# Optimization experiments

Hardware: AMD Instinct MI355X
Metric: run time of the kernel (lower is better)

Reference implementation:

```python
import jax, jax.numpy as jnp
import numpy as np

B, N, F_IN = 32, 512, 64
HEADS = (8, 8)
HIDS = (64, 64)
EDGE_P = 0.05  # graph density
NEG_SLOPE = 0.2
NEG_INF = -1e20


def setup_inputs() -> dict:
    key = jax.random.key(0)
    ks = jax.random.split(key, 8)
    x = jax.random.normal(ks[0], (B, N, F_IN), dtype=jnp.float32)
    adj = (jax.random.uniform(ks[1], (B, N, N)) < EDGE_P).astype(jnp.float32)
    adj = jnp.maximum(adj, adj.transpose(0, 2, 1))  # symmetric adjacency
    # mask = (batch, row): every (b, n) pair gets the masked softmax
    b_idx = jnp.repeat(jnp.arange(B, dtype=jnp.int32), N)   # [B*N]
    r_idx = jnp.tile(jnp.arange(N, dtype=jnp.int32), B)     # [B*N]
    # layer 0: f_in=64 -> f_out=64, H=8 ; layer 1: f_in=64*8=512 -> f_out=64, H=8
    W0 = jax.random.normal(ks[2], (F_IN, HIDS[0]), dtype=jnp.float32) / jnp.sqrt(jnp.float32(F_IN))
    a_src0 = jax.random.normal(ks[3], (HIDS[0], HEADS[0]), dtype=jnp.float32) / jnp.sqrt(jnp.float32(HIDS[0]))
    a_dst0 = jax.random.normal(ks[4], (HIDS[0], HEADS[0]), dtype=jnp.float32) / jnp.sqrt(jnp.float32(HIDS[0]))
    f_in1 = HIDS[0] * HEADS[0]
    W1 = jax.random.normal(ks[5], (f_in1, HIDS[1]), dtype=jnp.float32) / jnp.sqrt(jnp.float32(f_in1))
    a_src1 = jax.random.normal(ks[6], (HIDS[1], HEADS[1]), dtype=jnp.float32) / jnp.sqrt(jnp.float32(HIDS[1]))
    a_dst1 = jax.random.normal(ks[7], (HIDS[1], HEADS[1]), dtype=jnp.float32) / jnp.sqrt(jnp.float32(HIDS[1]))
    return dict(x=x, adj=adj, b_idx=b_idx, r_idx=r_idx,
                W0=W0, a_src0=a_src0, a_dst0=a_dst0,
                W1=W1, a_src1=a_src1, a_dst1=a_dst1)


def _gat_layer(x, adj, b_idx, r_idx, W, a_src, a_dst):
    # x: [B,N,f_in], adj: [B,N,N] (diag already set), W: [f_in,F], a_*: [F,H]
    hp = x @ W                                        # [B,N,F]
    s = jnp.einsum('bnf,fh->bhn', hp, a_src)          # attn_src
    d = jnp.einsum('bnf,fh->bhn', hp, a_dst)          # attn_dst
    attn = s[:, :, :, None] + d[:, :, None, :]        # [B,H,N,N]
    attn = jnp.where(attn >= 0, attn, NEG_SLOPE * attn)  # leaky_relu(0.2)
    attn = jnp.where(adj[:, None, :, :] == 0, 0.0, attn)  # masked_fill(adj==0, 0)
    rows = attn[b_idx, :, r_idx, :]                   # [K,H,N]
    rows = jnp.where(rows == 0.0, NEG_INF, rows)
    rows = jax.nn.softmax(rows, axis=-1)
    attn = attn.at[b_idx, :, r_idx, :].set(rows)
    return jnp.einsum('bhij,bjf->bhif', attn, hp)     # [B,H,N,F]


def reference(x, adj, b_idx, r_idx, W0, a_src0, a_dst0, W1, a_src1, a_dst1):
    Bn, Nn = x.shape[:2]
    # torch mutates adj in place: adj[batch,row,row] = 1 (self loops)
    adj = adj.at[b_idx, r_idx, r_idx].set(1.0)
    o = _gat_layer(x, adj, b_idx, r_idx, W0, a_src0, a_dst0)      # [B,H,N,F0]
    x1 = jax.nn.elu(o.transpose(0, 2, 1, 3).reshape(Bn, Nn, -1))  # [B,N,H*F0]
    o2 = _gat_layer(x1, adj, b_idx, r_idx, W1, a_src1, a_dst1)    # [B,H,N,F1]
    return o2.mean(axis=1)                                        # [B,N,F1]
```

## Files before the change

### kernel.cpp

```cpp
#include <hip/hip_runtime.h>
#include <hip/hip_bf16.h>
#include <math.h>

#define BB 32
#define NN 512

typedef _Float16 f16x8 __attribute__((ext_vector_type(8)));
typedef __fp16  fp16x2 __attribute__((ext_vector_type(2)));
typedef float f32x4 __attribute__((ext_vector_type(4)));

#define MFMA16(a, b, c) __builtin_amdgcn_mfma_f32_16x16x32_f16(a, b, c, 0, 0, 0)

union AF { f16x8 v; unsigned int u[4]; };

__device__ __forceinline__ void gload_lds16(const void* g, void* l) {
    __builtin_amdgcn_global_load_lds(
        (const __attribute__((address_space(1))) unsigned int*)g,
        (__attribute__((address_space(3))) unsigned int*)l, 16, 0, 0);
}
__device__ __forceinline__ void gload_lds4(const void* g, void* l) {
    __builtin_amdgcn_global_load_lds(
        (const __attribute__((address_space(1))) unsigned int*)g,
        (__attribute__((address_space(3))) unsigned int*)l, 4, 0, 0);
}

static __device__ __forceinline__ void epi16(
    const float* ctile, const float* asd_f, int row0, int t,
    float* __restrict__ s, float* __restrict__ dTg, _Float16* __restrict__ hpT,
    float* dmax_lds, float* __restrict__ pmax_out)
{
    int b = row0 >> 9, jb = row0 & 511;
    if (t < 128) {
        int rr = t >> 3, h = t & 7;
        float sv = 0.f, dv = 0.f;
#pragma unroll
        for (int f = 0; f < 64; ++f) {
            float hv = ctile[rr * 66 + f];
            sv = fmaf(hv, asd_f[f * 8 + h], sv);
            dv = fmaf(hv, asd_f[512 + f * 8 + h], dv);
        }
        s[((size_t)b * NN + jb + rr) * 8 + h] = sv;
        dTg[((size_t)b * 8 + h) * NN + jb + rr] = dv;
        dmax_lds[t] = dv;
    } else if (t < 256) {
        int t2 = t - 128;
        int f = t2 >> 1, jl = (t2 & 1) * 8;
        f16x8 hv;
#pragma unroll
        for (int e = 0; e < 8; ++e)
            hv[e] = (_Float16)ctile[(jl + e) * 66 + f];
        *(f16x8*)(hpT + ((size_t)b * 64 + f) * NN + jb + jl) = hv;
    }
    __syncthreads();
    if (t < 8) {
        float m = dmax_lds[t];
#pragma unroll
        for (int k = 1; k < 16; ++k) m = fmaxf(m, dmax_lds[t + 8 * k]);
        pmax_out[((size_t)b * 32 + (jb >> 4)) * 8 + t] = m;
    }
}

static __device__ __forceinline__ void epi32(
    const float* ctile, const float* asd_f, int row0, int t,
    float* __restrict__ s, float* __restrict__ dTg, _Float16* __restrict__ hpT,
    float* dmax_lds, float* __restrict__ pmax_out)
{
    int b = row0 >> 9, jb = row0 & 511;
    if (t < 256) {
        int rr = t >> 3, h = t & 7;
        float sv = 0.f, dv = 0.f;
#pragma unroll
        for (int f = 0; f < 64; ++f) {
            float hv = ctile[rr * 66 + f];
            sv = fmaf(hv, asd_f[f * 8 + h], sv);
            dv = fmaf(hv, asd_f[512 + f * 8 + h], dv);
        }
        s[((size_t)b * NN + jb + rr) * 8 + h] = sv;
        dTg[((size_t)b * 8 + h) * NN + jb + rr] = dv;
        dmax_lds[t] = dv;
    } else {
        int t2 = t - 256;
        int f = t2 >> 2, jl = (t2 & 3) * 8;
        f16x8 hv;
#pragma unroll
        for (int e = 0; e < 8; ++e)
            hv[e] = (_Float16)ctile[(jl + e) * 66 + f];
        *(f16x8*)(hpT + ((size_t)b * 64 + f) * NN + jb + jl) = hv;
    }
    __syncthreads();
    if (t < 8) {
        float m = dmax_lds[t];
#pragma unroll
        for (int k = 1; k < 32; ++k) m = fmaxf(m, dmax_lds[t + 8 * k]);
        pmax_out[((size_t)b * 16 + (jb >> 5)) * 8 + t] = m;
    }
}

__global__ __launch_bounds__(256) void k_front(
    const float* __restrict__ x, const float* __restrict__ W0,
    const float* __restrict__ W1, _Float16* __restrict__ W1T,
    const float* __restrict__ a_src, const float* __restrict__ a_dst,
    float* __restrict__ s, float* __restrict__ dTg, _Float16* __restrict__ hpT,
    float* __restrict__ pmax)
{
    __shared__ float ctile[16 * 66];
    __shared__ float asd_f[1024];
    __shared__ float dmax[128];
    int t = threadIdx.x, row0 = blockIdx.x * 16;
    int lane = t & 63, w = t >> 6, cn = lane & 15, rq = lane >> 4;

    if (blockIdx.x < 16) {
        int task = blockIdx.x * 256 + t;
        int n = task & 63, gabs = task >> 6;
        int c = gabs >> 3, g = gabs & 7;
        f16x8 hv;
#pragma unroll
        for (int e = 0; e < 8; ++e)
            hv[e] = (_Float16)W1[(size_t)(gabs * 8 + e) * 64 + n];
        *(f16x8*)(W1T + (size_t)n * 512 + c * 64 + (g ^ (n & 7)) * 8) = hv;
    }

    ((float4*)asd_f)[t] = (t < 128) ? ((const float4*)a_src)[t]
                                    : ((const float4*)a_dst)[t - 128];
    f32x4 acc;
#pragma unroll
    for (int e = 0; e < 4; ++e) acc[e] = 0.f;
    int nn0 = w * 16 + cn;
#pragma unroll
    for (int ks = 0; ks < 2; ++ks) {
        const float* xp = x + (size_t)(row0 + cn) * 64 + ks * 32 + rq * 8;
        float4 x0 = *(const float4*)xp, x1 = *(const float4*)(xp + 4);
        f16x8 ah = {(_Float16)x0.x, (_Float16)x0.y, (_Float16)x0.z, (_Float16)x0.w,
                    (_Float16)x1.x, (_Float16)x1.y, (_Float16)x1.z, (_Float16)x1.w};
        f16x8 bh;
#pragma unroll
        for (int e = 0; e < 8; ++e)
            bh[e] = (_Float16)W0[(size_t)((ks * 4 + rq) * 8 + e) * 64 + nn0];
        acc = MFMA16(ah, bh, acc);
    }
#pragma unroll
    for (int r = 0; r < 4; ++r)
        ctile[(rq * 4 + r) * 66 + w * 16 + cn] = acc[r];
    __syncthreads();
    epi16(ctile, asd_f, row0, t, s, dTg, hpT, dmax, pmax);
}

#define PBUILD(AOUT, SV, C0, CB, AVv, REL, DDv, Ev, Ebv)                \
    do {                                                                \
        _Pragma("unroll")                                               \
        for (int e = 0; e < 8; e += 2) {                                \
            float pA[2];                                                \
            _Pragma("unroll")                                           \
            for (int q = 0; q < 2; ++q) {                               \
                int ee = e + q;                                         \
                bool con = (AVv[ee] != 0.f) || (ee == (REL));           \
                float e0 = SV + DDv[ee];                                \
                float p0 = (e0 >= 0.f) ? (C0) * Ev[ee] : (CB) * Ebv[ee];\
                pA[q] = (con && e0 != 0.f) ? p0 : 0.f;                  \
            }                                                           \
            fp16x2 ka = __builtin_amdgcn_cvt_pkrtz(pA[0], pA[1]);       \
            AOUT.u[e >> 1] = __builtin_bit_cast(unsigned int, ka);      \
        }                                                               \
    } while (0)

template<int MODE>
__global__ __launch_bounds__(512, 4) void k_attn_fused(
    const float* __restrict__ s, const float* __restrict__ dTg,
    const float* __restrict__ pmaxd, const _Float16* __restrict__ hpT,
    const float* __restrict__ adj,
    const _Float16* __restrict__ W1T,
    const float* __restrict__ a_src, const float* __restrict__ a_dst,
    float* __restrict__ s_out, float* __restrict__ dTg_out,
    _Float16* __restrict__ hpT_out, float* __restrict__ pmax_out,
    float* __restrict__ o_f)
{
    __shared__ __align__(16) char smem[40960];
    char* bufP = smem;
    char* bufQ = smem + 18432;

    int blk = blockIdx.x;
    int vb = ((blk & 7) << 6) | (blk >> 3);
    int b = vb >> 4, i0 = (vb & 15) << 5;
    int row0 = vb * 32;
    int t = threadIdx.x, lane = t & 63, w = t >> 6;
    int cn = lane & 15, rq = lane >> 4;
    int myrow = i0 + cn;

    const _Float16* hb = hpT + (size_t)b * 64 * NN;
    int f0 = t >> 3, g0 = t & 7;
    const _Float16* hsrc = hb + (size_t)f0 * NN + ((g0 ^ (f0 & 7)) * 8);
    const float* dsrc = dTg + ((size_t)b * 8 + w) * NN + lane;
    int ar = t >> 4, ag = t & 15;
    const float* asrc = adj + (size_t)(row0 + ar) * NN + (((ag ^ (ar & 7))) << 2);

#define STAGE(BUF, JC)                                                   \
    do {                                                                 \
        gload_lds16(hsrc + (JC), (_Float16*)(BUF) + (w << 9));           \
        gload_lds4(dsrc + (JC), (float*)((BUF) + 8192) + (w << 6));      \
        gload_lds16(asrc + (JC), (float*)((BUF) + 10240) + (w << 8));    \
    } while (0)

    STAGE(bufP, 0);

    constexpr int NT = (MODE == 0) ? 32 : 16;
    float md = pmaxd[((size_t)b * NT + (lane & (NT - 1))) * 8 + w];
#pragma unroll
    for (int off = NT >> 1; off; off >>= 1) md = fmaxf(md, __shfl_xor(md, off));

    float svA = s[((size_t)b * NN + myrow) * 8 + w];
    float svB = s[((size_t)b * NN + myrow + 16) * 8 + w];
    float MA = fmaxf(svA + md, 0.f);
    float MB = fmaxf(svB + md, 0.f);
    float c0A = __expf(svA + md - MA), cbA = __expf(0.2f * (svA + md) - MA);
    float c0B = __expf(svB + md - MB), cbB = __expf(0.2f * (svB + md) - MB);
    int rq8 = rq * 8;

    f16x8 ones;
#pragma unroll
    for (int e = 0; e < 8; ++e) ones[e] = (_Float16)1.0f;

    f32x4 accA[4], accB[4], accrsA, accrsB;
#pragma unroll
    for (int e = 0; e < 4; ++e) { accrsA[e] = 0.f; accrsB[e] = 0.f; }
#pragma unroll
    for (int ft = 0; ft < 4; ++ft)
#pragma unroll
        for (int e = 0; e < 4; ++e) { accA[ft][e] = 0.f; accB[ft][e] = 0.f; }

    __syncthreads();

    for (int jcx = 0; jcx < 8; ++jcx) {
        int jc = jcx * 64;
        char* cur = (jcx & 1) ? bufQ : bufP;
        char* nxt = (jcx & 1) ? bufP : bufQ;
        if (jcx < 7) STAGE(nxt, jc + 64);
        const _Float16* hTc = (const _Float16*)cur;
        const float* ddl = (const float*)(cur + 8192) + (w << 6);
        const float* adl = (const float*)(cur + 10240);
        const float* arA = adl + cn * 64;
        const float* arB = adl + (16 + cn) * 64;
        int xA = cn & 7;
        float* Et = (float*)(smem + 36864) + (w << 7);
        {
            float ddj = ddl[lane];
            Et[lane]      = __expf(ddj - md);
            Et[lane + 64] = __expf(0.2f * (ddj - md));
        }
        asm volatile("s_waitcnt lgkmcnt(0)" ::: "memory");
#pragma unroll
        for (int ks = 0; ks < 2; ++ks) {
            int jo = ks * 32 + rq8;
            float dd[8], avA[8], avB[8], Ev[8], Ebv[8];
            *(float4*)&dd[0] = *(const float4*)(ddl + jo);
            *(float4*)&dd[4] = *(const float4*)(ddl + jo + 4);
            *(float4*)&Ev[0]  = *(const float4*)(Et + jo);
            *(float4*)&Ev[4]  = *(const float4*)(Et + jo + 4);
            *(float4*)&Ebv[0] = *(const float4*)(Et + 64 + jo);
            *(float4*)&Ebv[4] = *(const float4*)(Et + 64 + jo + 4);
            int G0 = jo >> 2;
            *(float4*)&avA[0] = *(const float4*)(arA + ((G0 ^ xA) << 2));
            *(float4*)&avA[4] = *(const float4*)(arA + (((G0 + 1) ^ xA) << 2));
            *(float4*)&avB[0] = *(const float4*)(arB + ((G0 ^ xA) << 2));
            *(float4*)&avB[4] = *(const float4*)(arB + (((G0 + 1) ^ xA) << 2));
            int relA = myrow - (jc + jo);
            int relB = relA + 16;
            AF aA, aB;
            PBUILD(aA, svA, c0A, cbA, avA, relA, dd, Ev, Ebv);
            PBUILD(aB, svB, c0B, cbB, avB, relB, dd, Ev, Ebv);
            __builtin_amdgcn_s_setprio(1);
            accrsA = MFMA16(aA.v, ones, accrsA);
            accrsB = MFMA16(aB.v, ones, accrsB);
#pragma unroll
            for (int ft = 0; ft < 4; ++ft) {
                int f = ft * 16 + cn;
                f16x8 bh = *(const f16x8*)&hTc[f * 64 + (((ks * 4 + rq) ^ (f & 7)) * 8)];
                accA[ft] = MFMA16(aA.v, bh, accA[ft]);
                accB[ft] = MFMA16(aB.v, bh, accB[ft]);
            }
            __builtin_amdgcn_s_setprio(0);
        }
        __syncthreads();
    }
#undef STAGE

    float invrA[4], invrB[4];
#pragma unroll
    for (int r = 0; r < 4; ++r) {
        invrA[r] = 1.0f / accrsA[r];
        invrB[r] = 1.0f / accrsB[r];
    }

    if (MODE == 0) {
        _Float16* x1all = (_Float16*)smem;
#pragma unroll
        for (int rt = 0; rt < 2; ++rt)
#pragma unroll
            for (int ft = 0; ft < 4; ++ft)
#pragma unroll
                for (int r = 0; r < 4; ++r) {
                    int il = rt * 16 + rq * 4 + r;
                    float v = rt ? accB[ft][r] * invrB[r]
                                 : accA[ft][r] * invrA[r];
                    v = v > 0.f ? v : __expf(v) - 1.f;
                    int f = ft * 16 + cn;
                    x1all[w * 2048 + il * 64 + (((f >> 3) ^ (il & 7)) * 8) + (f & 7)] =
                        (_Float16)v;
                }
        __syncthreads();
        f32x4 g1A, g1B;
#pragma unroll
        for (int e = 0; e < 4; ++e) { g1A[e] = 0.f; g1B[e] = 0.f; }
        int nn = (w & 3) * 16 + cn, kh = w >> 2;
        const _Float16* wb = W1T + (size_t)nn * 512;
#pragma unroll
        for (int kc2 = 0; kc2 < 4; ++kc2) {
            int kc = kh * 4 + kc2;
#pragma unroll
            for (int ks = 0; ks < 2; ++ks) {
                f16x8 bh = *(const f16x8*)(wb + kc * 64 +
                                           (((ks * 4 + rq) ^ (nn & 7)) * 8));
                f16x8 ahA = *(const f16x8*)&x1all[kc * 2048 + cn * 64 +
                                                  (((ks * 4 + rq) ^ (cn & 7)) * 8)];
                f16x8 ahB = *(const f16x8*)&x1all[kc * 2048 + (16 + cn) * 64 +
                                                  (((ks * 4 + rq) ^ (cn & 7)) * 8)];
                g1A = MFMA16(ahA, bh, g1A);
                g1B = MFMA16(ahB, bh, g1B);
            }
        }
        __syncthreads();
        float* ct = (float*)smem;
        float* asd_f = (float*)(smem + 33280);
        float* dmax = (float*)(smem + 37376);
#pragma unroll
        for (int r = 0; r < 4; ++r) {
            ct[kh * 2112 + (rq * 4 + r) * 66 + nn] = g1A[r];
            ct[kh * 2112 + (16 + rq * 4 + r) * 66 + nn] = g1B[r];
        }
        if (t < 256)
            ((float4*)asd_f)[t] = (t < 128) ? ((const float4*)a_src)[t]
                                            : ((const float4*)a_dst)[t - 128];
        __syncthreads();
        for (int idx = t; idx < 2112; idx += 512) ct[idx] += ct[2112 + idx];
        __syncthreads();
        epi32(ct, asd_f, row0, t, s_out, dTg_out, hpT_out, dmax, pmax_out);
    } else {
        float* red = (float*)smem;
#pragma unroll
        for (int ph = 0; ph < 2; ++ph) {
            if ((w >> 2) == ph) {
#pragma unroll
                for (int rt = 0; rt < 2; ++rt)
#pragma unroll
                    for (int ft = 0; ft < 4; ++ft)
#pragma unroll
                        for (int r = 0; r < 4; ++r) {
                            int il = rt * 16 + rq * 4 + r;
                            float v = rt ? accB[ft][r] * invrB[r]
                                         : accA[ft][r] * invrA[r];
                            int off = (w & 3) * 2048 + il * 64 + ft * 16 + cn;
                            if (ph == 0) red[off] = v;
                            else         red[off] += v;
                        }
            }
            __syncthreads();
        }
#pragma unroll
        for (int u = 0; u < 4; ++u) {
            int idx = t + u * 512;
            int il = idx >> 6, f = idx & 63;
            float sum = red[il * 64 + f] + red[2048 + il * 64 + f]
                      + red[4096 + il * 64 + f] + red[6144 + il * 64 + f];
            o_f[((size_t)b * NN + i0 + il) * 64 + f] = sum * 0.125f;
        }
    }
}

extern "C" void kernel_launch(void* const* d_in, const int* in_sizes, int n_in,
                              void* d_out, int out_size, void* d_ws, size_t ws_size,
                              hipStream_t stream) {
    const float* x      = (const float*)d_in[0];
    const float* adj    = (const float*)d_in[1];
    const float* W0     = (const float*)d_in[4];
    const float* a_src0 = (const float*)d_in[5];
    const float* a_dst0 = (const float*)d_in[6];
    const float* W1     = (const float*)d_in[7];
    const float* a_src1 = (const float*)d_in[8];
    const float* a_dst1 = (const float*)d_in[9];
    float* out = (float*)d_out;

    float* ws = (float*)d_ws;
    const size_t R = (size_t)BB * NN;
    const size_t BHN = (size_t)BB * 8 * NN;
    float* s0    = ws;
    float* dTg0  = s0 + R * 8;
    float* s1    = dTg0 + BHN;
    float* dTg1  = s1 + R * 8;
    float* pmax0 = dTg1 + BHN;
    float* pmax1 = pmax0 + 8192;
    _Float16* hp0T = (_Float16*)(pmax1 + 4096);
    _Float16* hp1T = hp0T + (size_t)BB * 64 * NN;
    _Float16* W1T  = hp1T + (size_t)BB * 64 * NN;

    k_front<<<1024, 256, 0, stream>>>(x, W0, W1, W1T, a_src0, a_dst0,
                                      s0, dTg0, hp0T, pmax0);
    k_attn_fused<0><<<512, 512, 0, stream>>>(s0, dTg0, pmax0, hp0T, adj,
                                             W1T, a_src1, a_dst1,
                                             s1, dTg1, hp1T, pmax1, nullptr);
    k_attn_fused<1><<<512, 512, 0, stream>>>(s1, dTg1, pmax1, hp1T, adj,
                                             nullptr, nullptr, nullptr,
                                             nullptr, nullptr, nullptr, nullptr, out);
}
```

Before: 153.3 us.

## Replace LDS double-buffered staging with direct global loads in attention kernel

```diff
diff --git a/kernel.cpp b/kernel.cpp
--- a/kernel.cpp
+++ b/kernel.cpp
@@ -12,17 +12,6 @@
 #define MFMA16(a, b, c) __builtin_amdgcn_mfma_f32_16x16x32_f16(a, b, c, 0, 0, 0)
 
 union AF { f16x8 v; unsigned int u[4]; };
-
-__device__ __forceinline__ void gload_lds16(const void* g, void* l) {
-    __builtin_amdgcn_global_load_lds(
-        (const __attribute__((address_space(1))) unsigned int*)g,
-        (__attribute__((address_space(3))) unsigned int*)l, 16, 0, 0);
-}
-__device__ __forceinline__ void gload_lds4(const void* g, void* l) {
-    __builtin_amdgcn_global_load_lds(
-        (const __attribute__((address_space(1))) unsigned int*)g,
-        (__attribute__((address_space(3))) unsigned int*)l, 4, 0, 0);
-}
 
 static __device__ __forceinline__ void epi16(
     const float* ctile, const float* asd_f, int row0, int t,
@@ -175,8 +164,6 @@
     float* __restrict__ o_f)
 {
     __shared__ __align__(16) char smem[40960];
-    char* bufP = smem;
-    char* bufQ = smem + 18432;
 
     int blk = blockIdx.x;
     int vb = ((blk & 7) << 6) | (blk >> 3);
@@ -187,20 +174,9 @@
     int myrow = i0 + cn;
 
     const _Float16* hb = hpT + (size_t)b * 64 * NN;
-    int f0 = t >> 3, g0 = t & 7;
-    const _Float16* hsrc = hb + (size_t)f0 * NN + ((g0 ^ (f0 & 7)) * 8);
-    const float* dsrc = dTg + ((size_t)b * 8 + w) * NN + lane;
-    int ar = t >> 4, ag = t & 15;
-    const float* asrc = adj + (size_t)(row0 + ar) * NN + (((ag ^ (ar & 7))) << 2);
-
-#define STAGE(BUF, JC)                                                   \
-    do {                                                                 \
-        gload_lds16(hsrc + (JC), (_Float16*)(BUF) + (w << 9));           \
-        gload_lds4(dsrc + (JC), (float*)((BUF) + 8192) + (w << 6));      \
-        gload_lds16(asrc + (JC), (float*)((BUF) + 10240) + (w << 8));    \
-    } while (0)
-
-    STAGE(bufP, 0);
+    const float* ddg  = dTg + ((size_t)b * 8 + w) * NN;
+    const float* arAg = adj + ((size_t)b * NN + myrow) * NN;
+    const float* arBg = arAg + (size_t)16 * NN;
 
     constexpr int NT = (MODE == 0) ? 32 : 16;
     float md = pmaxd[((size_t)b * NT + (lane & (NT - 1))) * 8 + w];
@@ -227,22 +203,13 @@
 #pragma unroll
         for (int e = 0; e < 4; ++e) { accA[ft][e] = 0.f; accB[ft][e] = 0.f; }
 
-    __syncthreads();
-
+    float* Et = (float*)(smem + 36864) + (w << 7);
+
+#pragma unroll 2
     for (int jcx = 0; jcx < 8; ++jcx) {
         int jc = jcx * 64;
-        char* cur = (jcx & 1) ? bufQ : bufP;
-        char* nxt = (jcx & 1) ? bufP : bufQ;
-        if (jcx < 7) STAGE(nxt, jc + 64);
-        const _Float16* hTc = (const _Float16*)cur;
-        const float* ddl = (const float*)(cur + 8192) + (w << 6);
-        const float* adl = (const float*)(cur + 10240);
-        const float* arA = adl + cn * 64;
-        const float* arB = adl + (16 + cn) * 64;
-        int xA = cn & 7;
-        float* Et = (float*)(smem + 36864) + (w << 7);
         {
-            float ddj = ddl[lane];
+            float ddj = ddg[jc + lane];
             Et[lane]      = __expf(ddj - md);
             Et[lane + 64] = __expf(0.2f * (ddj - md));
         }
@@ -251,17 +218,16 @@
         for (int ks = 0; ks < 2; ++ks) {
             int jo = ks * 32 + rq8;
             float dd[8], avA[8], avB[8], Ev[8], Ebv[8];
-            *(float4*)&dd[0] = *(const float4*)(ddl + jo);
-            *(float4*)&dd[4] = *(const float4*)(ddl + jo + 4);
+            *(float4*)&dd[0]  = *(const float4*)(ddg + jc + jo);
+            *(float4*)&dd[4]  = *(const float4*)(ddg + jc + jo + 4);
             *(float4*)&Ev[0]  = *(const float4*)(Et + jo);
             *(float4*)&Ev[4]  = *(const float4*)(Et + jo + 4);
             *(float4*)&Ebv[0] = *(const float4*)(Et + 64 + jo);
             *(float4*)&Ebv[4] = *(const float4*)(Et + 64 + jo + 4);
-            int G0 = jo >> 2;
-            *(float4*)&avA[0] = *(const float4*)(arA + ((G0 ^ xA) << 2));
-            *(float4*)&avA[4] = *(const float4*)(arA + (((G0 + 1) ^ xA) << 2));
-            *(float4*)&avB[0] = *(const float4*)(arB + ((G0 ^ xA) << 2));
-            *(float4*)&avB[4] = *(const float4*)(arB + (((G0 + 1) ^ xA) << 2));
+            *(float4*)&avA[0] = *(const float4*)(arAg + jc + jo);
+            *(float4*)&avA[4] = *(const float4*)(arAg + jc + jo + 4);
+            *(float4*)&avB[0] = *(const float4*)(arBg + jc + jo);
+            *(float4*)&avB[4] = *(const float4*)(arBg + jc + jo + 4);
             int relA = myrow - (jc + jo);
             int relB = relA + 16;
             AF aA, aB;
@@ -272,16 +238,13 @@
             accrsB = MFMA16(aB.v, ones, accrsB);
 #pragma unroll
             for (int ft = 0; ft < 4; ++ft) {
-                int f = ft * 16 + cn;
-                f16x8 bh = *(const f16x8*)&hTc[f * 64 + (((ks * 4 + rq) ^ (f & 7)) * 8)];
+                f16x8 bh = *(const f16x8*)(hb + (size_t)(ft * 16 + cn) * NN + jc + jo);
                 accA[ft] = MFMA16(aA.v, bh, accA[ft]);
                 accB[ft] = MFMA16(aB.v, bh, accB[ft]);
             }
             __builtin_amdgcn_s_setprio(0);
         }
-        __syncthreads();
-    }
-#undef STAGE
+    }
 
     float invrA[4], invrB[4];
 #pragma unroll
```

After: 223.9 us. 46.0% more time.
